# Optimization experiments

Measured on AMD Instinct MI355X. Metric: run time of the kernel, lower is better.

## Reference

```python
import jax, jax.numpy as jnp
import numpy as np

N_HEADS = 16


def setup_inputs() -> dict:
    key = jax.random.key(0)
    k1, k2, k3 = jax.random.split(key, 3)
    n_embed = 1024
    b, t = 4, 2048
    x = jax.random.normal(k1, (b, t, n_embed), dtype=jnp.float32)
    # Linear weights stored as [in, out]; y = x @ W + b (same math as torch Linear).
    Wqkv = jax.random.normal(k2, (n_embed, 3 * n_embed), dtype=jnp.float32) * (n_embed ** -0.5)
    bqkv = jnp.zeros((3 * n_embed,), dtype=jnp.float32)
    Wout = jax.random.normal(k3, (n_embed, n_embed), dtype=jnp.float32) * (n_embed ** -0.5)
    bout = jnp.zeros((n_embed,), dtype=jnp.float32)
    return {"x": x, "Wqkv": Wqkv, "bqkv": bqkv, "Wout": Wout, "bout": bout}


def reference(x, Wqkv, bqkv, Wout, bout):
    b, t, n_embed = x.shape
    hs = n_embed // N_HEADS
    qkv = x @ Wqkv + bqkv  # [b, t, 3*n_embed]
    q, k, v = jnp.split(qkv, 3, axis=-1)
    # b t (h hs) -> b h t hs
    def to_heads(u):
        return u.reshape(b, t, N_HEADS, hs).transpose(0, 2, 1, 3)
    q, k, v = to_heads(q), to_heads(k), to_heads(v)
    scale = 1.0 / jnp.sqrt(jnp.asarray(hs, dtype=x.dtype))
    scores = jnp.einsum('bhqd,bhkd->bhqk', q, k) * scale  # [b, h, t, t]
    causal = jnp.tril(jnp.ones((t, t), dtype=bool))
    scores = jnp.where(causal, scores, jnp.finfo(scores.dtype).min)
    attn = jax.nn.softmax(scores, axis=-1)
    out = jnp.einsum('bhqk,bhkd->bhqd', attn, v)  # [b, h, t, hs]
    out = out.transpose(0, 2, 1, 3).reshape(b, t, n_embed)  # b h t hs -> b t (h hs)
    return out @ Wout + bout
```

## Files before the change

kernel.cpp:

```cpp
#include <hip/hip_runtime.h>
#include <hip/hip_bf16.h>
#include <stdint.h>

typedef unsigned short u16;
typedef __bf16 bf16x8 __attribute__((ext_vector_type(8)));
typedef float f32x4 __attribute__((ext_vector_type(4)));
typedef u16 ushort8 __attribute__((ext_vector_type(8)));
typedef short short4v __attribute__((ext_vector_type(4)));

__device__ __forceinline__ u16 f2bf(float f) {
    unsigned int u = __builtin_bit_cast(unsigned int, f);
    u += 0x7fffu + ((u >> 16) & 1u);
    return (u16)(u >> 16);
}

#define MFMA16(a, b, c) __builtin_amdgcn_mfma_f32_16x16x32_bf16( \
    __builtin_bit_cast(bf16x8, a), __builtin_bit_cast(bf16x8, b), c, 0, 0, 0)

#if defined(__has_builtin)
#if __has_builtin(__builtin_amdgcn_exp2f)
#define EXP2(x) __builtin_amdgcn_exp2f(x)
#endif
#endif
#ifndef EXP2
#define EXP2(x) __expf((x) * 0.69314718f)
#endif

__device__ __forceinline__ void async16(void* lds, const void* g) {
    __builtin_amdgcn_global_load_lds(
        (const __attribute__((address_space(1))) unsigned int*)(uintptr_t)g,
        (__attribute__((address_space(3))) unsigned int*)(unsigned int)(uintptr_t)lds,
        16, 0, 0);
}

__global__ __launch_bounds__(256) void convert_bf16(
    const float* __restrict__ src, u16* __restrict__ dst)
{
    int i = blockIdx.x * 256 + threadIdx.x;
    float4 f0 = ((const float4*)src)[i * 2];
    float4 f1 = ((const float4*)src)[i * 2 + 1];
    ushort8 v;
    v[0]=f2bf(f0.x); v[1]=f2bf(f0.y); v[2]=f2bf(f0.z); v[3]=f2bf(f0.w);
    v[4]=f2bf(f1.x); v[5]=f2bf(f1.y); v[6]=f2bf(f1.z); v[7]=f2bf(f1.w);
    ((ushort8*)dst)[i] = v;
}

__global__ __launch_bounds__(256) void transpose_convert(
    const float* __restrict__ src, u16* __restrict__ dst, int N, int K)
{
    __shared__ u16 T[64][68];
    const int k0 = blockIdx.x * 64, n0 = blockIdx.y * 64;
    const int tid = threadIdx.x;
    const int rr = tid >> 4, cc = (tid & 15) * 4;
    #pragma unroll
    for (int rnd = 0; rnd < 4; ++rnd) {
        int r = rr + rnd * 16;
        float4 f = *(const float4*)&src[(size_t)(k0 + r) * N + n0 + cc];
        u16 v[4] = {f2bf(f.x), f2bf(f.y), f2bf(f.z), f2bf(f.w)};
        *(unsigned long long*)&T[r][cc] = *(unsigned long long*)v;
    }
    __syncthreads();
    #pragma unroll
    for (int rnd = 0; rnd < 4; ++rnd) {
        int rn = rr + rnd * 16;
        u16 v[4];
        #pragma unroll
        for (int j = 0; j < 4; ++j) v[j] = T[cc + j][rn];
        *(unsigned long long*)&dst[(size_t)(n0 + rn) * K + k0 + cc] =
            *(unsigned long long*)v;
    }
}

#define KT_N 16

__device__ __forceinline__ void stage_tile256(
    const u16* __restrict__ A, const u16* __restrict__ Bt,
    u16* Lb, int m0, int n0, int k0, int w, int grow, int gchunk)
{
    #pragma unroll
    for (int r = 0; r < 4; ++r) {
        int rb = w * 4 + r;
        async16(Lb + rb * 512,
                A + (size_t)(m0 + rb * 8 + grow) * 1024 + k0 + gchunk * 8);
    }
    #pragma unroll
    for (int r = 0; r < 2; ++r) {
        int rb = w * 2 + r;
        async16(Lb + 16384 + rb * 512,
                Bt + (size_t)(n0 + rb * 8 + grow) * 1024 + k0 + gchunk * 8);
    }
}

__device__ __forceinline__ void gemm_mainloop256(
    const u16* __restrict__ A, const u16* __restrict__ Bt,
    u16* L, int m0, int n0, int tid, f32x4 acc[4][4])
{
    const int lane = tid & 63, w = tid >> 6;
    const int lr = lane & 15, quad = lane >> 4;
    const int wm = w >> 1, wn = w & 1;
    const int grow = lane & 7, gchunk = lane >> 3;

    stage_tile256(A, Bt, L,         m0, n0, 0,  w, grow, gchunk);
    stage_tile256(A, Bt, L + 24576, m0, n0, 64, w, grow, gchunk);

    u16* Lc = L;
    u16* Ls = L + 49152;
    u16* const Lend = L + 73728;

    for (int t = 0; t < KT_N; ++t) {
        if (t < KT_N - 2)
            stage_tile256(A, Bt, Ls, m0, n0, (t + 2) * 64, w, grow, gchunk);

        if (t < KT_N - 2)       asm volatile("s_waitcnt vmcnt(12)" ::: "memory");
        else if (t == KT_N - 2) asm volatile("s_waitcnt vmcnt(6)"  ::: "memory");
        else                    asm volatile("s_waitcnt vmcnt(0)"  ::: "memory");
        __builtin_amdgcn_s_barrier();
        asm volatile("" ::: "memory");

        const u16* As = Lc;
        const u16* Bs = Lc + 16384;
        __builtin_amdgcn_s_setprio(1);
        #pragma unroll
        for (int kk = 0; kk < 2; ++kk) {
            ushort8 a[4], b[4];
            #pragma unroll
            for (int mt = 0; mt < 4; ++mt) {
                int rb = wm * 8 + mt * 2 + (lr >> 3);
                a[mt] = *(const ushort8*)&As[rb * 512 + (kk * 4 + quad) * 64 + (lr & 7) * 8];
            }
            #pragma unroll
            for (int nt = 0; nt < 4; ++nt) {
                int rb = wn * 8 + nt * 2 + (lr >> 3);
                b[nt] = *(const ushort8*)&Bs[rb * 512 + (kk * 4 + quad) * 64 + (lr & 7) * 8];
            }
            #pragma unroll
            for (int mt = 0; mt < 4; ++mt)
                #pragma unroll
                for (int nt = 0; nt < 4; ++nt)
                    acc[mt][nt] = MFMA16(a[mt], b[nt], acc[mt][nt]);
        }
        __builtin_amdgcn_s_setprio(0);
        asm volatile("" ::: "memory");
        __builtin_amdgcn_s_barrier();
        asm volatile("" ::: "memory");

        Lc += 24576; if (Lc == Lend) Lc = L;
        Ls += 24576; if (Ls == Lend) Ls = L;
    }
}

__global__ __launch_bounds__(512, 2) void qkv_gemm(
    const u16* __restrict__ xb, const u16* __restrict__ Wt,
    const float* __restrict__ bias, u16* __restrict__ qkvb)
{
    __shared__ u16 L[73728];
    const int m0 = blockIdx.x * 256, n0 = blockIdx.y * 128;
    const int tid = threadIdx.x;
    f32x4 acc[4][4] = {};
    gemm_mainloop256(xb, Wt, L, m0, n0, tid, acc);

    const int lane = tid & 63, w = tid >> 6;
    const int lr = lane & 15, quad = lane >> 4;
    const int wm = w >> 1, wn = w & 1;
    const int which = n0 >> 10;
    float bv[4];
    #pragma unroll
    for (int nt = 0; nt < 4; ++nt) bv[nt] = bias[n0 + wn * 64 + nt * 16 + lr];

    if (which == 2) {
        u16* vT = qkvb + (size_t)2 * 8388608;
        #pragma unroll
        for (int nt = 0; nt < 4; ++nt) {
            int n = n0 + wn * 64 + nt * 16 + lr;
            int hh = (n >> 6) & 15, d = n & 63;
            #pragma unroll
            for (int mt = 0; mt < 4; ++mt) {
                int mbase = m0 + wm * 64 + mt * 16 + quad * 4;
                int b_idx = mbase >> 11, t0 = mbase & 2047;
                short4v o4;
                #pragma unroll
                for (int reg = 0; reg < 4; ++reg)
                    o4[reg] = (short)f2bf(acc[mt][nt][reg] + bv[nt]);
                *(short4v*)&vT[((size_t)(b_idx * 16 + hh) * 64 + d) * 2048 + t0] = o4;
            }
        }
    } else {
        u16* dst = qkvb + (size_t)which * 8388608;
        #pragma unroll
        for (int mt = 0; mt < 4; ++mt)
          #pragma unroll
          for (int nt = 0; nt < 4; ++nt) {
            int n = n0 + wn * 64 + nt * 16 + lr;
            int hh = (n >> 6) & 15, d = n & 63;
            #pragma unroll
            for (int reg = 0; reg < 4; ++reg) {
                int m = m0 + wm * 64 + mt * 16 + quad * 4 + reg;
                int b_idx = m >> 11, t_idx = m & 2047;
                dst[(((size_t)(b_idx * 16 + hh) * 2048 + t_idx) << 6) + d] =
                    f2bf(acc[mt][nt][reg] + bv[nt]);
            }
          }
    }
}

__global__ __launch_bounds__(512, 2) void out_gemm(
    const u16* __restrict__ A, const u16* __restrict__ Wt,
    const float* __restrict__ bias, float* __restrict__ out)
{
    __shared__ u16 L[73728];
    const int m0 = blockIdx.x * 256, n0 = blockIdx.y * 128;
    const int tid = threadIdx.x;
    f32x4 acc[4][4] = {};
    gemm_mainloop256(A, Wt, L, m0, n0, tid, acc);

    const int lane = tid & 63, w = tid >> 6;
    const int lr = lane & 15, quad = lane >> 4;
    const int wm = w >> 1, wn = w & 1;
    float bv[4];
    #pragma unroll
    for (int nt = 0; nt < 4; ++nt) bv[nt] = bias[n0 + wn * 64 + nt * 16 + lr];
    #pragma unroll
    for (int mt = 0; mt < 4; ++mt)
      #pragma unroll
      for (int nt = 0; nt < 4; ++nt)
        #pragma unroll
        for (int reg = 0; reg < 4; ++reg) {
            int m = m0 + wm * 64 + mt * 16 + quad * 4 + reg;
            int n = n0 + wn * 64 + nt * 16 + lr;
            out[(size_t)m * 1024 + n] = acc[mt][nt][reg] + bv[nt];
        }
}

__global__ __launch_bounds__(256) void attn_kernel(
    const u16* __restrict__ qkvb, u16* __restrict__ o_ws)
{
    const int orig = blockIdx.x + 16 * (blockIdx.y + 16 * blockIdx.z);
    const int work = (orig & 7) * 128 + (orig >> 3);
    const int p = work & 15, h = (work >> 4) & 15, b = work >> 8;
    const size_t bh = (size_t)(b * 16 + h) * 131072;
    const u16* Qb = qkvb + bh;
    const u16* Kb = qkvb + 8388608 + bh;
    const u16* Vt = qkvb + 2 * 8388608 + bh;
    __shared__ u16 Ks[2][4096];
    __shared__ u16 Vts[4096];
    __shared__ u16 Ps[64 * 72];
    const int tid = threadIdx.x, lane = tid & 63, w = tid >> 6;
    const int lr = lane & 15, quad = lane >> 4;
    const int grow = lane & 7, gchunk = lane >> 3;
    const float kscale = 0.125f * 1.44269504f;

    for (int pass = 0; pass < 2; ++pass) {
        const int qt = pass ? (31 - p) : p;
        ushort8 qf[2];
        {
            const u16* qr = Qb + (size_t)(qt * 64 + w * 16 + lr) * 64 + quad * 8;
            qf[0] = *(const ushort8*)qr;
            qf[1] = *(const ushort8*)(qr + 32);
        }
        f32x4 o_acc[4] = {};
        float m_i = -1e30f, l_i = 0.f;
        const int qrow = w * 16 + lr;
        const int bsrc = (lane & 48) + ((lane >> 4) << 2);

        __syncthreads();
        #pragma unroll
        for (int r = 0; r < 2; ++r) {
            int rb = w * 2 + r;
            async16(&Ks[0][rb * 512], Kb + (size_t)(rb * 8 + grow) * 64 + gchunk * 8);
        }

        for (int kt = 0; kt <= qt; ++kt) {
            const int buf = kt & 1;
            __syncthreads();

            #pragma unroll
            for (int r = 0; r < 2; ++r) {
                int rb = w * 2 + r;
                if (kt < qt)
                    async16(&Ks[buf ^ 1][rb * 512],
                            Kb + (size_t)((kt + 1) * 64 + rb * 8 + grow) * 64 + gchunk * 8);
                async16(&Vts[rb * 512],
                        Vt + (size_t)(rb * 8 + grow) * 2048 + kt * 64 + gchunk * 8);
            }

            f32x4 s[4] = {};
            #pragma unroll
            for (int nt = 0; nt < 4; ++nt)
                #pragma unroll
                for (int kk = 0; kk < 2; ++kk) {
                    ushort8 bb = *(ushort8*)&Ks[buf][(nt * 2 + (lr >> 3)) * 512 +
                                                     (kk * 4 + quad) * 64 + (lr & 7) * 8];
                    s[nt] = MFMA16(bb, qf[kk], s[nt]);
                }
            if (kt == qt) {
                #pragma unroll
                for (int nt = 0; nt < 4; ++nt)
                    #pragma unroll
                    for (int reg = 0; reg < 4; ++reg) {
                        int kc = nt * 16 + quad * 4 + reg;
                        s[nt][reg] = (kc > qrow) ? -1e30f : s[nt][reg] * kscale;
                    }
            } else {
                #pragma unroll
                for (int nt = 0; nt < 4; ++nt)
                    #pragma unroll
                    for (int reg = 0; reg < 4; ++reg) s[nt][reg] *= kscale;
            }
            float mx = -1e30f;
            #pragma unroll
            for (int nt = 0; nt < 4; ++nt)
                #pragma unroll
                for (int reg = 0; reg < 4; ++reg) mx = fmaxf(mx, s[nt][reg]);
            mx = fmaxf(mx, __shfl_xor(mx, 16, 64));
            mx = fmaxf(mx, __shfl_xor(mx, 32, 64));
            if (!__all(mx <= m_i + 8.0f)) {
                float mnew = fmaxf(m_i, mx);
                float alpha = EXP2(m_i - mnew);
                m_i = mnew;
                l_i *= alpha;
                #pragma unroll
                for (int reg = 0; reg < 4; ++reg) {
                    float ar = __shfl(alpha, bsrc + reg, 64);
                    #pragma unroll
                    for (int dt = 0; dt < 4; ++dt) o_acc[dt][reg] *= ar;
                }
            }
            float p4[4][4];
            float rs = 0.f;
            #pragma unroll
            for (int nt = 0; nt < 4; ++nt)
                #pragma unroll
                for (int reg = 0; reg < 4; ++reg) {
                    float pv = EXP2(s[nt][reg] - m_i);
                    p4[nt][reg] = pv;
                    rs += pv;
                }
            rs += __shfl_xor(rs, 16, 64);
            rs += __shfl_xor(rs, 32, 64);
            l_i += rs;
            #pragma unroll
            for (int nt = 0; nt < 4; ++nt) {
                u16 v4[4];
                #pragma unroll
                for (int reg = 0; reg < 4; ++reg) v4[reg] = f2bf(p4[nt][reg]);
                *(unsigned long long*)&Ps[qrow * 72 + nt * 16 + quad * 4] =
                    *(unsigned long long*)v4;
            }

            __syncthreads();

            #pragma unroll
            for (int kk = 0; kk < 2; ++kk) {
                ushort8 pa = *(ushort8*)&Ps[(w * 16 + lr) * 72 + kk * 32 + quad * 8];
                #pragma unroll
                for (int dt = 0; dt < 4; ++dt) {
                    ushort8 vb = *(ushort8*)&Vts[(dt * 2 + (lr >> 3)) * 512 +
                                                 (kk * 4 + quad) * 64 + (lr & 7) * 8];
                    o_acc[dt] = MFMA16(pa, vb, o_acc[dt]);
                }
            }
        }

        float rinv = 1.0f / l_i;
        float rl[4];
        #pragma unroll
        for (int reg = 0; reg < 4; ++reg) rl[reg] = __shfl(rinv, bsrc + reg, 64);
        #pragma unroll
        for (int dt = 0; dt < 4; ++dt)
            #pragma unroll
            for (int reg = 0; reg < 4; ++reg) {
                int row = w * 16 + quad * 4 + reg;
                int tq = qt * 64 + row;
                o_ws[((size_t)(b * 2048 + tq) << 10) + h * 64 + dt * 16 + lr] =
                    f2bf(o_acc[dt][reg] * rl[reg]);
            }
    }
}

extern "C" void kernel_launch(void* const* d_in, const int* in_sizes, int n_in,
                              void* d_out, int out_size, void* d_ws, size_t ws_size,
                              hipStream_t stream)
{
    const float* x    = (const float*)d_in[0];
    const float* Wqkv = (const float*)d_in[1];
    const float* bqkv = (const float*)d_in[2];
    const float* Wout = (const float*)d_in[3];
    const float* bout = (const float*)d_in[4];
    float* out = (float*)d_out;

    u16* qkvb = (u16*)d_ws;
    u16* xb   = qkvb + (size_t)3 * 8388608;
    u16* wT   = qkvb + (size_t)4 * 8388608;
    u16* attn_o = xb;

    convert_bf16<<<4096, 256, 0, stream>>>(x, xb);
    transpose_convert<<<dim3(16, 48), 256, 0, stream>>>(Wqkv, wT, 3072, 1024);
    qkv_gemm<<<dim3(32, 24), 512, 0, stream>>>(xb, wT, bqkv, qkvb);
    attn_kernel<<<dim3(16, 16, 4), 256, 0, stream>>>(qkvb, attn_o);
    transpose_convert<<<dim3(16, 16), 256, 0, stream>>>(Wout, wT, 1024, 1024);
    out_gemm<<<dim3(32, 8), 512, 0, stream>>>(attn_o, wT, bout, out);
}
```

Before: 279.9 us.

## Retile QKV GEMM to 256x192 blocks with split double-buffered A/B staging

The QKV projection GEMM now uses 256x192 output tiles (512 blocks instead of 768) with a new mainloop: 2x4 wave layout, 8x3 MFMA accumulators per wave, double-buffered LDS, and A and B tile loads issued at different points in the iteration. Each k-step is split into four MFMA phases separated by barriers and setprio. The aim is to raise arithmetic intensity per block and hide global-load latency behind MFMA work. In exchange it adds more barriers and register pressure, and the epilogue must handle a tile that crosses Q/K/V boundaries per column.

```diff
diff --git a/kernel.cpp b/kernel.cpp
--- a/kernel.cpp
+++ b/kernel.cpp
@@ -71,11 +71,12 @@
     }
 }
 
-#define KT_N 16
-
-__device__ __forceinline__ void stage_tile256(
-    const u16* __restrict__ A, const u16* __restrict__ Bt,
-    u16* Lb, int m0, int n0, int k0, int w, int grow, int gchunk)
+#define QK_TILES 16
+#define QBUF 28672
+
+__device__ __forceinline__ void stageA192(
+    const u16* __restrict__ A, u16* Lb, int m0, int k0,
+    int w, int grow, int gchunk)
 {
     #pragma unroll
     for (int r = 0; r < 4; ++r) {
@@ -83,6 +84,182 @@
         async16(Lb + rb * 512,
                 A + (size_t)(m0 + rb * 8 + grow) * 1024 + k0 + gchunk * 8);
     }
+}
+
+__device__ __forceinline__ void stageB192(
+    const u16* __restrict__ Bt, u16* Lb, int n0, int k0,
+    int w, int grow, int gchunk)
+{
+    #pragma unroll
+    for (int r = 0; r < 3; ++r) {
+        int rb = w * 3 + r;
+        async16(Lb + 16384 + rb * 512,
+                Bt + (size_t)(n0 + rb * 8 + grow) * 1024 + k0 + gchunk * 8);
+    }
+}
+
+__device__ __forceinline__ void gemm_mainloop192(
+    const u16* __restrict__ A, const u16* __restrict__ Bt,
+    u16* L, int m0, int n0, int tid, f32x4 acc[8][3])
+{
+    const int lane = tid & 63, w = tid >> 6;
+    const int lr = lane & 15, quad = lane >> 4;
+    const int wm = w >> 2, wn = w & 3;
+    const int grow = lane & 7, gchunk = lane >> 3;
+    const int arb = wm * 16 + (lr >> 3);
+    const int brb = wn * 6 + (lr >> 3);
+    const int foff = (lr & 7) * 8;
+
+    stageA192(A, L, m0, 0, w, grow, gchunk);
+    stageB192(Bt, L, n0, 0, w, grow, gchunk);
+    asm volatile("s_waitcnt vmcnt(0)" ::: "memory");
+    __builtin_amdgcn_s_barrier();
+    asm volatile("" ::: "memory");
+
+    #pragma unroll 2
+    for (int t = 0; t < QK_TILES; ++t) {
+        const u16* As = L + (t & 1) * QBUF;
+        const u16* Bs = As + 16384;
+        ushort8 a03[4], a47[4], b[3];
+
+        if (t + 1 < QK_TILES) {
+            stageA192(A, L + ((t + 1) & 1) * QBUF, m0, (t + 1) * 64,
+                      w, grow, gchunk);
+            asm volatile("s_waitcnt vmcnt(4)" ::: "memory");
+        } else {
+            asm volatile("s_waitcnt vmcnt(0)" ::: "memory");
+        }
+        __builtin_amdgcn_s_barrier();
+        asm volatile("" ::: "memory");
+        #pragma unroll
+        for (int nt = 0; nt < 3; ++nt)
+            b[nt] = *(const ushort8*)&Bs[(brb + nt * 2) * 512 + quad * 64 + foff];
+        #pragma unroll
+        for (int mt = 0; mt < 4; ++mt)
+            a03[mt] = *(const ushort8*)&As[(arb + mt * 2) * 512 + quad * 64 + foff];
+        asm volatile("s_waitcnt lgkmcnt(0)" ::: "memory");
+        __builtin_amdgcn_sched_barrier(0);
+        __builtin_amdgcn_s_setprio(1);
+        #pragma unroll
+        for (int mt = 0; mt < 4; ++mt)
+            #pragma unroll
+            for (int nt = 0; nt < 3; ++nt)
+                acc[mt][nt] = MFMA16(a03[mt], b[nt], acc[mt][nt]);
+        __builtin_amdgcn_s_setprio(0);
+        __builtin_amdgcn_s_barrier();
+
+        #pragma unroll
+        for (int mt = 0; mt < 4; ++mt)
+            a47[mt] = *(const ushort8*)&As[(arb + (mt + 4) * 2) * 512 + quad * 64 + foff];
+        __builtin_amdgcn_s_barrier();
+        asm volatile("s_waitcnt lgkmcnt(0)" ::: "memory");
+        __builtin_amdgcn_sched_barrier(0);
+        __builtin_amdgcn_s_setprio(1);
+        #pragma unroll
+        for (int mt = 0; mt < 4; ++mt)
+            #pragma unroll
+            for (int nt = 0; nt < 3; ++nt)
+                acc[mt + 4][nt] = MFMA16(a47[mt], b[nt], acc[mt + 4][nt]);
+        __builtin_amdgcn_s_setprio(0);
+        __builtin_amdgcn_s_barrier();
+
+        if (t + 1 < QK_TILES)
+            stageB192(Bt, L + ((t + 1) & 1) * QBUF, n0, (t + 1) * 64,
+                      w, grow, gchunk);
+        #pragma unroll
+        for (int nt = 0; nt < 3; ++nt)
+            b[nt] = *(const ushort8*)&Bs[(brb + nt * 2) * 512 + 256 + quad * 64 + foff];
+        #pragma unroll
+        for (int mt = 0; mt < 4; ++mt)
+            a03[mt] = *(const ushort8*)&As[(arb + mt * 2) * 512 + 256 + quad * 64 + foff];
+        __builtin_amdgcn_s_barrier();
+        asm volatile("s_waitcnt lgkmcnt(0)" ::: "memory");
+        __builtin_amdgcn_sched_barrier(0);
+        __builtin_amdgcn_s_setprio(1);
+        #pragma unroll
+        for (int mt = 0; mt < 4; ++mt)
+            #pragma unroll
+            for (int nt = 0; nt < 3; ++nt)
+                acc[mt][nt] = MFMA16(a03[mt], b[nt], acc[mt][nt]);
+        __builtin_amdgcn_s_setprio(0);
+        __builtin_amdgcn_s_barrier();
+
+        #pragma unroll
+        for (int mt = 0; mt < 4; ++mt)
+            a47[mt] = *(const ushort8*)&As[(arb + (mt + 4) * 2) * 512 + 256 + quad * 64 + foff];
+        __builtin_amdgcn_s_barrier();
+        asm volatile("s_waitcnt lgkmcnt(0)" ::: "memory");
+        __builtin_amdgcn_sched_barrier(0);
+        __builtin_amdgcn_s_setprio(1);
+        #pragma unroll
+        for (int mt = 0; mt < 4; ++mt)
+            #pragma unroll
+            for (int nt = 0; nt < 3; ++nt)
+                acc[mt + 4][nt] = MFMA16(a47[mt], b[nt], acc[mt + 4][nt]);
+        __builtin_amdgcn_s_setprio(0);
+        __builtin_amdgcn_s_barrier();
+        asm volatile("" ::: "memory");
+    }
+}
+
+__global__ __launch_bounds__(512, 2) void qkv_gemm(
+    const u16* __restrict__ xb, const u16* __restrict__ Wt,
+    const float* __restrict__ bias, u16* __restrict__ qkvb)
+{
+    __shared__ u16 L[2 * QBUF];
+    const int m0 = blockIdx.x * 256, n0 = blockIdx.y * 192;
+    const int tid = threadIdx.x;
+    f32x4 acc[8][3] = {};
+    gemm_mainloop192(xb, Wt, L, m0, n0, tid, acc);
+
+    const int lane = tid & 63, w = tid >> 6;
+    const int lr = lane & 15, quad = lane >> 4;
+    const int wm = w >> 2, wn = w & 3;
+    u16* vT = qkvb + (size_t)2 * 8388608;
+
+    #pragma unroll
+    for (int nt = 0; nt < 3; ++nt) {
+        int n = n0 + wn * 48 + nt * 16 + lr;
+        int which = n >> 10;
+        int hh = (n >> 6) & 15, d = n & 63;
+        float bvn = bias[n];
+        if (which == 2) {
+            #pragma unroll
+            for (int mt = 0; mt < 8; ++mt) {
+                int mbase = m0 + wm * 128 + mt * 16 + quad * 4;
+                int b_idx = mbase >> 11, t0 = mbase & 2047;
+                short4v o4;
+                #pragma unroll
+                for (int reg = 0; reg < 4; ++reg)
+                    o4[reg] = (short)f2bf(acc[mt][nt][reg] + bvn);
+                *(short4v*)&vT[((size_t)(b_idx * 16 + hh) * 64 + d) * 2048 + t0] = o4;
+            }
+        } else {
+            u16* dst = qkvb + (size_t)which * 8388608;
+            #pragma unroll
+            for (int mt = 0; mt < 8; ++mt) {
+                #pragma unroll
+                for (int reg = 0; reg < 4; ++reg) {
+                    int m = m0 + wm * 128 + mt * 16 + quad * 4 + reg;
+                    int b_idx = m >> 11, t_idx = m & 2047;
+                    dst[(((size_t)(b_idx * 16 + hh) * 2048 + t_idx) << 6) + d] =
+                        f2bf(acc[mt][nt][reg] + bvn);
+                }
+            }
+        }
+    }
+}
+
+__device__ __forceinline__ void stage_tile256(
+    const u16* __restrict__ A, const u16* __restrict__ Bt,
+    u16* Lb, int m0, int n0, int k0, int w, int grow, int gchunk)
+{
+    #pragma unroll
+    for (int r = 0; r < 4; ++r) {
+        int rb = w * 4 + r;
+        async16(Lb + rb * 512,
+                A + (size_t)(m0 + rb * 8 + grow) * 1024 + k0 + gchunk * 8);
+    }
     #pragma unroll
     for (int r = 0; r < 2; ++r) {
         int rb = w * 2 + r;
@@ -107,13 +284,13 @@
     u16* Ls = L + 49152;
     u16* const Lend = L + 73728;
 
-    for (int t = 0; t < KT_N; ++t) {
-        if (t < KT_N - 2)
+    for (int t = 0; t < QK_TILES; ++t) {
+        if (t < QK_TILES - 2)
             stage_tile256(A, Bt, Ls, m0, n0, (t + 2) * 64, w, grow, gchunk);
 
-        if (t < KT_N - 2)       asm volatile("s_waitcnt vmcnt(12)" ::: "memory");
-        else if (t == KT_N - 2) asm volatile("s_waitcnt vmcnt(6)"  ::: "memory");
-        else                    asm volatile("s_waitcnt vmcnt(0)"  ::: "memory");
+        if (t < QK_TILES - 2)       asm volatile("s_waitcnt vmcnt(12)" ::: "memory");
+        else if (t == QK_TILES - 2) asm volatile("s_waitcnt vmcnt(6)"  ::: "memory");
+        else                        asm volatile("s_waitcnt vmcnt(0)"  ::: "memory");
         __builtin_amdgcn_s_barrier();
         asm volatile("" ::: "memory");
 
@@ -146,60 +323,6 @@
 
         Lc += 24576; if (Lc == Lend) Lc = L;
         Ls += 24576; if (Ls == Lend) Ls = L;
-    }
-}
-
-__global__ __launch_bounds__(512, 2) void qkv_gemm(
-    const u16* __restrict__ xb, const u16* __restrict__ Wt,
-    const float* __restrict__ bias, u16* __restrict__ qkvb)
-{
-    __shared__ u16 L[73728];
-    const int m0 = blockIdx.x * 256, n0 = blockIdx.y * 128;
-    const int tid = threadIdx.x;
-    f32x4 acc[4][4] = {};
-    gemm_mainloop256(xb, Wt, L, m0, n0, tid, acc);
-
-    const int lane = tid & 63, w = tid >> 6;
-    const int lr = lane & 15, quad = lane >> 4;
-    const int wm = w >> 1, wn = w & 1;
-    const int which = n0 >> 10;
-    float bv[4];
-    #pragma unroll
-    for (int nt = 0; nt < 4; ++nt) bv[nt] = bias[n0 + wn * 64 + nt * 16 + lr];
-
-    if (which == 2) {
-        u16* vT = qkvb + (size_t)2 * 8388608;
-        #pragma unroll
-        for (int nt = 0; nt < 4; ++nt) {
-            int n = n0 + wn * 64 + nt * 16 + lr;
-            int hh = (n >> 6) & 15, d = n & 63;
-            #pragma unroll
-            for (int mt = 0; mt < 4; ++mt) {
-                int mbase = m0 + wm * 64 + mt * 16 + quad * 4;
-                int b_idx = mbase >> 11, t0 = mbase & 2047;
-                short4v o4;
-                #pragma unroll
-                for (int reg = 0; reg < 4; ++reg)
-                    o4[reg] = (short)f2bf(acc[mt][nt][reg] + bv[nt]);
-                *(short4v*)&vT[((size_t)(b_idx * 16 + hh) * 64 + d) * 2048 + t0] = o4;
-            }
-        }
-    } else {
-        u16* dst = qkvb + (size_t)which * 8388608;
-        #pragma unroll
-        for (int mt = 0; mt < 4; ++mt)
-          #pragma unroll
-          for (int nt = 0; nt < 4; ++nt) {
-            int n = n0 + wn * 64 + nt * 16 + lr;
-            int hh = (n >> 6) & 15, d = n & 63;
-            #pragma unroll
-            for (int reg = 0; reg < 4; ++reg) {
-                int m = m0 + wm * 64 + mt * 16 + quad * 4 + reg;
-                int b_idx = m >> 11, t_idx = m & 2047;
-                dst[(((size_t)(b_idx * 16 + hh) * 2048 + t_idx) << 6) + d] =
-                    f2bf(acc[mt][nt][reg] + bv[nt]);
-            }
-          }
     }
 }
 
@@ -395,7 +518,7 @@
 
     convert_bf16<<<4096, 256, 0, stream>>>(x, xb);
     transpose_convert<<<dim3(16, 48), 256, 0, stream>>>(Wqkv, wT, 3072, 1024);
-    qkv_gemm<<<dim3(32, 24), 512, 0, stream>>>(xb, wT, bqkv, qkvb);
+    qkv_gemm<<<dim3(32, 16), 512, 0, stream>>>(xb, wT, bqkv, qkvb);
     attn_kernel<<<dim3(16, 16, 4), 256, 0, stream>>>(qkvb, attn_o);
     transpose_convert<<<dim3(16, 16), 256, 0, stream>>>(Wout, wT, 1024, 1024);
     out_gemm<<<dim3(32, 8), 512, 0, stream>>>(attn_o, wT, bout, out);
```

New measurement: 280.3 us. About the same (+0.1%).

## Rewrite QKV GEMM with 256x256 tiles, K=32 double-buffered pipeline

Applied to the files above, without the earlier changes.

Replaces the QKV projection GEMM with a new mainloop that uses 256x256 output tiles per block (8 waves in a 2x4 grid, 8x4 MFMA tiles each), K-step 32 and a two-stage LDS double buffer, halving the grid in N. The larger tile raises arithmetic intensity per loaded byte and shrinks LDS use, which could allow more resident blocks. It also splits the A-fragment loads into two halves with explicit lgkmcnt waits so LDS reads overlap MFMAs. The costs are more accumulator registers, which may lower occupancy or cause spills, and a barrier every 32-wide K step instead of every 64.

```diff
diff --git a/kernel.cpp b/kernel.cpp
--- a/kernel.cpp
+++ b/kernel.cpp
@@ -71,7 +71,150 @@
     }
 }
 
-#define KT_N 16
+#define NT32 32
+#define BUF32 16384
+
+__device__ __forceinline__ void stage32(
+    const u16* __restrict__ A, const u16* __restrict__ Bt,
+    u16* Lb, int m0, int n0, int k0, int w, int lane)
+{
+    const int rbl = lane >> 5;
+    const int chunk = (lane >> 3) & 3;
+    const int row = lane & 7;
+    #pragma unroll
+    for (int r = 0; r < 2; ++r) {
+        int rb = w * 4 + r * 2 + rbl;
+        async16(Lb + (w * 4 + r * 2) * 256,
+                A + (size_t)(m0 + rb * 8 + row) * 1024 + k0 + chunk * 8);
+    }
+    #pragma unroll
+    for (int r = 0; r < 2; ++r) {
+        int rb = w * 4 + r * 2 + rbl;
+        async16(Lb + 8192 + (w * 4 + r * 2) * 256,
+                Bt + (size_t)(n0 + rb * 8 + row) * 1024 + k0 + chunk * 8);
+    }
+}
+
+__device__ __forceinline__ void gemm_mainloop32(
+    const u16* __restrict__ A, const u16* __restrict__ Bt,
+    u16* L, int m0, int n0, int tid, f32x4 acc[8][4])
+{
+    const int lane = tid & 63, w = tid >> 6;
+    const int lr = lane & 15, quad = lane >> 4;
+    const int wm = w >> 2, wn = w & 3;
+    const int arb = wm * 16 + (lr >> 3);
+    const int brb = wn * 8 + (lr >> 3);
+    const int foff = quad * 64 + (lr & 7) * 8;
+
+    stage32(A, Bt, L, m0, n0, 0, w, lane);
+    asm volatile("s_waitcnt vmcnt(0)" ::: "memory");
+    __builtin_amdgcn_s_barrier();
+    asm volatile("" ::: "memory");
+
+    #pragma unroll 2
+    for (int t = 0; t < NT32; ++t) {
+        const u16* As = L + (t & 1) * BUF32;
+        const u16* Bs = As + 8192;
+
+        if (t + 1 < NT32) {
+            stage32(A, Bt, L + ((t + 1) & 1) * BUF32, m0, n0, (t + 1) * 32,
+                    w, lane);
+            asm volatile("s_waitcnt vmcnt(4)" ::: "memory");
+        } else {
+            asm volatile("s_waitcnt vmcnt(0)" ::: "memory");
+        }
+        __builtin_amdgcn_s_barrier();
+        asm volatile("" ::: "memory");
+
+        ushort8 b[4], a03[4], a47[4];
+        #pragma unroll
+        for (int nt = 0; nt < 4; ++nt)
+            b[nt] = *(const ushort8*)&Bs[(brb + nt * 2) * 256 + foff];
+        #pragma unroll
+        for (int mt = 0; mt < 4; ++mt)
+            a03[mt] = *(const ushort8*)&As[(arb + mt * 2) * 256 + foff];
+        __builtin_amdgcn_sched_barrier(0);
+        #pragma unroll
+        for (int mt = 0; mt < 4; ++mt)
+            a47[mt] = *(const ushort8*)&As[(arb + (mt + 4) * 2) * 256 + foff];
+        asm volatile("s_waitcnt lgkmcnt(4)" ::: "memory");
+        __builtin_amdgcn_sched_barrier(0);
+        __builtin_amdgcn_s_setprio(1);
+        #pragma unroll
+        for (int mt = 0; mt < 4; ++mt)
+            #pragma unroll
+            for (int nt = 0; nt < 4; ++nt)
+                acc[mt][nt] = MFMA16(a03[mt], b[nt], acc[mt][nt]);
+        __builtin_amdgcn_s_setprio(0);
+        asm volatile("s_waitcnt lgkmcnt(0)" ::: "memory");
+        __builtin_amdgcn_sched_barrier(0);
+        __builtin_amdgcn_s_setprio(1);
+        #pragma unroll
+        for (int mt = 0; mt < 4; ++mt)
+            #pragma unroll
+            for (int nt = 0; nt < 4; ++nt)
+                acc[mt + 4][nt] = MFMA16(a47[mt], b[nt], acc[mt + 4][nt]);
+        __builtin_amdgcn_s_setprio(0);
+        __builtin_amdgcn_s_barrier();
+        asm volatile("" ::: "memory");
+    }
+}
+
+__global__ __launch_bounds__(512, 2) void qkv_gemm(
+    const u16* __restrict__ xb, const u16* __restrict__ Wt,
+    const float* __restrict__ bias, u16* __restrict__ qkvb)
+{
+    __shared__ u16 L[2 * BUF32];
+    const int m0 = blockIdx.x * 256, n0 = blockIdx.y * 256;
+    const int tid = threadIdx.x;
+    f32x4 acc[8][4] = {};
+    gemm_mainloop32(xb, Wt, L, m0, n0, tid, acc);
+
+    const int lane = tid & 63, w = tid >> 6;
+    const int lr = lane & 15, quad = lane >> 4;
+    const int wm = w >> 2, wn = w & 3;
+    const int which = n0 >> 10;
+    float bv[4];
+    #pragma unroll
+    for (int nt = 0; nt < 4; ++nt) bv[nt] = bias[n0 + wn * 64 + nt * 16 + lr];
+
+    if (which == 2) {
+        u16* vT = qkvb + (size_t)2 * 8388608;
+        #pragma unroll
+        for (int nt = 0; nt < 4; ++nt) {
+            int n = n0 + wn * 64 + nt * 16 + lr;
+            int hh = (n >> 6) & 15, d = n & 63;
+            #pragma unroll
+            for (int mt = 0; mt < 8; ++mt) {
+                int mbase = m0 + wm * 128 + mt * 16 + quad * 4;
+                int b_idx = mbase >> 11, t0 = mbase & 2047;
+                short4v o4;
+                #pragma unroll
+                for (int reg = 0; reg < 4; ++reg)
+                    o4[reg] = (short)f2bf(acc[mt][nt][reg] + bv[nt]);
+                *(short4v*)&vT[((size_t)(b_idx * 16 + hh) * 64 + d) * 2048 + t0] = o4;
+            }
+        }
+    } else {
+        u16* dst = qkvb + (size_t)which * 8388608;
+        #pragma unroll
+        for (int mt = 0; mt < 8; ++mt)
+          #pragma unroll
+          for (int nt = 0; nt < 4; ++nt) {
+            int n = n0 + wn * 64 + nt * 16 + lr;
+            int hh = (n >> 6) & 15, d = n & 63;
+            #pragma unroll
+            for (int reg = 0; reg < 4; ++reg) {
+                int m = m0 + wm * 128 + mt * 16 + quad * 4 + reg;
+                int b_idx = m >> 11, t_idx = m & 2047;
+                dst[(((size_t)(b_idx * 16 + hh) * 2048 + t_idx) << 6) + d] =
+                    f2bf(acc[mt][nt][reg] + bv[nt]);
+            }
+          }
+    }
+}
+
+#define KT16 16
 
 __device__ __forceinline__ void stage_tile256(
     const u16* __restrict__ A, const u16* __restrict__ Bt,
@@ -107,12 +250,12 @@
     u16* Ls = L + 49152;
     u16* const Lend = L + 73728;
 
-    for (int t = 0; t < KT_N; ++t) {
-        if (t < KT_N - 2)
+    for (int t = 0; t < KT16; ++t) {
+        if (t < KT16 - 2)
             stage_tile256(A, Bt, Ls, m0, n0, (t + 2) * 64, w, grow, gchunk);
 
-        if (t < KT_N - 2)       asm volatile("s_waitcnt vmcnt(12)" ::: "memory");
-        else if (t == KT_N - 2) asm volatile("s_waitcnt vmcnt(6)"  ::: "memory");
+        if (t < KT16 - 2)       asm volatile("s_waitcnt vmcnt(12)" ::: "memory");
+        else if (t == KT16 - 2) asm volatile("s_waitcnt vmcnt(6)"  ::: "memory");
         else                    asm volatile("s_waitcnt vmcnt(0)"  ::: "memory");
         __builtin_amdgcn_s_barrier();
         asm volatile("" ::: "memory");
@@ -146,60 +289,6 @@
 
         Lc += 24576; if (Lc == Lend) Lc = L;
         Ls += 24576; if (Ls == Lend) Ls = L;
-    }
-}
-
-__global__ __launch_bounds__(512, 2) void qkv_gemm(
-    const u16* __restrict__ xb, const u16* __restrict__ Wt,
-    const float* __restrict__ bias, u16* __restrict__ qkvb)
-{
-    __shared__ u16 L[73728];
-    const int m0 = blockIdx.x * 256, n0 = blockIdx.y * 128;
-    const int tid = threadIdx.x;
-    f32x4 acc[4][4] = {};
-    gemm_mainloop256(xb, Wt, L, m0, n0, tid, acc);
-
-    const int lane = tid & 63, w = tid >> 6;
-    const int lr = lane & 15, quad = lane >> 4;
-    const int wm = w >> 1, wn = w & 1;
-    const int which = n0 >> 10;
-    float bv[4];
-    #pragma unroll
-    for (int nt = 0; nt < 4; ++nt) bv[nt] = bias[n0 + wn * 64 + nt * 16 + lr];
-
-    if (which == 2) {
-        u16* vT = qkvb + (size_t)2 * 8388608;
-        #pragma unroll
-        for (int nt = 0; nt < 4; ++nt) {
-            int n = n0 + wn * 64 + nt * 16 + lr;
-            int hh = (n >> 6) & 15, d = n & 63;
-            #pragma unroll
-            for (int mt = 0; mt < 4; ++mt) {
-                int mbase = m0 + wm * 64 + mt * 16 + quad * 4;
-                int b_idx = mbase >> 11, t0 = mbase & 2047;
-                short4v o4;
-                #pragma unroll
-                for (int reg = 0; reg < 4; ++reg)
-                    o4[reg] = (short)f2bf(acc[mt][nt][reg] + bv[nt]);
-                *(short4v*)&vT[((size_t)(b_idx * 16 + hh) * 64 + d) * 2048 + t0] = o4;
-            }
-        }
-    } else {
-        u16* dst = qkvb + (size_t)which * 8388608;
-        #pragma unroll
-        for (int mt = 0; mt < 4; ++mt)
-          #pragma unroll
-          for (int nt = 0; nt < 4; ++nt) {
-            int n = n0 + wn * 64 + nt * 16 + lr;
-            int hh = (n >> 6) & 15, d = n & 63;
-            #pragma unroll
-            for (int reg = 0; reg < 4; ++reg) {
-                int m = m0 + wm * 64 + mt * 16 + quad * 4 + reg;
-                int b_idx = m >> 11, t_idx = m & 2047;
-                dst[(((size_t)(b_idx * 16 + hh) * 2048 + t_idx) << 6) + d] =
-                    f2bf(acc[mt][nt][reg] + bv[nt]);
-            }
-          }
     }
 }
 
@@ -395,7 +484,7 @@
 
     convert_bf16<<<4096, 256, 0, stream>>>(x, xb);
     transpose_convert<<<dim3(16, 48), 256, 0, stream>>>(Wqkv, wT, 3072, 1024);
-    qkv_gemm<<<dim3(32, 24), 512, 0, stream>>>(xb, wT, bqkv, qkvb);
+    qkv_gemm<<<dim3(32, 12), 512, 0, stream>>>(xb, wT, bqkv, qkvb);
     attn_kernel<<<dim3(16, 16, 4), 256, 0, stream>>>(qkvb, attn_o);
     transpose_convert<<<dim3(16, 16), 256, 0, stream>>>(Wout, wT, 1024, 1024);
     out_gemm<<<dim3(32, 8), 512, 0, stream>>>(attn_o, wT, bout, out);
```

After: 274.0 us. -2.1%, faster.
